# Optimization experiments

Measured on AMD Instinct MI355X. Metric: run time of the kernel, lower is better.

Reference implementation:

```python
import jax, jax.numpy as jnp
import numpy as np

EMB = 128
HEADS = 8
B = 8
T = 2048


def setup_inputs() -> dict:
    key = jax.random.key(0)
    ks = jax.random.split(key, 6)
    x = jax.random.normal(ks[0], (B, T, EMB), dtype=jnp.float32)
    # torch Linear(emb, heads*emb, bias=False): store as (in, out) so y = x @ W
    scale = 1.0 / np.sqrt(EMB)
    Wq = jax.random.uniform(ks[1], (EMB, HEADS * EMB), jnp.float32, -scale, scale)
    Wk = jax.random.uniform(ks[2], (EMB, HEADS * EMB), jnp.float32, -scale, scale)
    Wv = jax.random.uniform(ks[3], (EMB, HEADS * EMB), jnp.float32, -scale, scale)
    so = 1.0 / np.sqrt(HEADS * EMB)
    Wo = jax.random.uniform(ks[4], (HEADS * EMB, EMB), jnp.float32, -so, so)
    bo = jax.random.uniform(ks[5], (EMB,), jnp.float32, -so, so)
    return {"x": x, "Wq": Wq, "Wk": Wk, "Wv": Wv, "Wo": Wo, "bo": bo}


def reference(x, Wq, Wk, Wv, Wo, bo):
    b, t, e = x.shape
    h = HEADS
    q = (x @ Wq).reshape(b, t, h, e)  # [b,t,h,e]
    k = (x @ Wk).reshape(b, t, h, e)
    v = (x @ Wv).reshape(b, t, h, e)
    # scores: [b,h,q,k], scaled by sqrt(e) (per-head dim == emb here)
    scores = jnp.einsum('bqhe,bkhe->bhqk', q, k) / jnp.sqrt(jnp.asarray(e, x.dtype))
    attn = jax.nn.softmax(scores, axis=-1)
    out = jnp.einsum('bhqk,bkhe->bqhe', attn, v).reshape(b, t, h * e)
    return out @ Wo + bo
```

## Files before the change

kernel.cpp:

```cpp
#include <hip/hip_runtime.h>

using bf16x8 = __attribute__((ext_vector_type(8))) short;
using f32x4  = __attribute__((ext_vector_type(4))) float;
using f32x16 = __attribute__((ext_vector_type(16))) float;

__device__ __forceinline__ ushort f2bf(float f) {
    union { float f; unsigned int u; } c; c.f = f;
    unsigned int u = c.u;
    u = (u + 0x7fffu + ((u >> 16) & 1u)) >> 16;
    return (ushort)u;
}

#if defined(__has_builtin)
#if __has_builtin(__builtin_amdgcn_cvt_pk_bf16_f32)
#define HAS_PK_BF16 1
#endif
#if __has_builtin(__builtin_amdgcn_permlane32_swap)
#define HAS_PL32 1
#endif
#endif
__device__ __forceinline__ unsigned int pkbf(float a, float b) {
#ifdef HAS_PK_BF16
    typedef __bf16 bf2 __attribute__((ext_vector_type(2)));
    union { bf2 v; unsigned int u; } cv;
    cv.v = __builtin_amdgcn_cvt_pk_bf16_f32(a, b);
    return cv.u;
#else
    return (unsigned int)f2bf(a) | ((unsigned int)f2bf(b) << 16);
#endif
}

__device__ __forceinline__ void pl32swap(unsigned &a, unsigned &b) {
#ifdef HAS_PL32
    typedef unsigned uint2v __attribute__((ext_vector_type(2)));
    uint2v r = __builtin_amdgcn_permlane32_swap(a, b, false, false);
    a = r.x; b = r.y;
#else
    asm volatile("v_permlane32_swap_b32 %0, %1" : "+v"(a), "+v"(b));
#endif
}

__device__ __forceinline__ void dma16(const ushort* g, ushort* l) {
    __builtin_amdgcn_global_load_lds(
        (const __attribute__((address_space(1))) unsigned int*)g,
        (__attribute__((address_space(3))) unsigned int*)l, 16, 0, 0);
}

constexpr int BB   = 8;
constexpr int HH   = 8;
constexpr int TT   = 2048;
constexpr int DD   = 128;
#define C2F (0.08838834764831845f * 1.4426950408889634f)

__global__ void prep_kernel(const float* __restrict__ x,
                            const float* __restrict__ Wq, const float* __restrict__ Wk,
                            const float* __restrict__ Wv, const float* __restrict__ Wo,
                            ushort* __restrict__ xb, ushort* __restrict__ WqkvT,
                            ushort* __restrict__ WoT) {
    int t = blockIdx.x * 256 + threadIdx.x;
    if (t < 524288) {
        float4 v = ((const float4*)x)[t];
        ushort4 o;
        o.x = f2bf(v.x); o.y = f2bf(v.y); o.z = f2bf(v.z); o.w = f2bf(v.w);
        ((ushort4*)xb)[t] = o;
    } else if (t < 524288 + 393216) {
        int i = t - 524288;
        int j = i >> 7, kk = i & 127;
        const float* W = (j < 1024) ? Wq : ((j < 2048) ? Wk : Wv);
        int jj = j & 1023;
        WqkvT[j * 128 + kk] = f2bf(W[kk * 1024 + jj]);
    } else {
        int i = t - 917504;
        int e = i >> 10, kk = i & 1023;
        WoT[e * 1024 + kk] = f2bf(Wo[kk * 128 + e]);
    }
}

__global__ __launch_bounds__(256, 2)
void qkv_gemm(const ushort* __restrict__ xb, const ushort* __restrict__ WqkvT,
              ushort* __restrict__ q, ushort* __restrict__ k, ushort* __restrict__ vt) {
    __shared__ ushort Al[128 * 136];
    __shared__ ushort Bl[128 * 136];
    const int tid = threadIdx.x;
    const int n0 = blockIdx.x * 128, m0 = blockIdx.y * 128;

    for (int s = tid; s < 2048; s += 256) {
        int row = s >> 4, oct = s & 15;
        *(uint4*)&Al[row * 136 + oct * 8] = *(const uint4*)&xb[m0 * 128 + s * 8];
        *(uint4*)&Bl[row * 136 + oct * 8] = *(const uint4*)&WqkvT[n0 * 128 + s * 8];
    }
    __syncthreads();

    const int w = tid >> 6, lane = tid & 63, l15 = lane & 15, g = lane >> 4;
    const int wm = (w & 1) * 64, wn = (w >> 1) * 64;
    f32x4 acc[4][4] = {};

#pragma unroll
    for (int ks = 0; ks < 4; ks++) {
        bf16x8 af[4], bfr[4];
#pragma unroll
        for (int mb = 0; mb < 4; mb++)
            af[mb] = *(const bf16x8*)&Al[(wm + mb * 16 + l15) * 136 + ks * 32 + g * 8];
#pragma unroll
        for (int nb = 0; nb < 4; nb++)
            bfr[nb] = *(const bf16x8*)&Bl[(wn + nb * 16 + l15) * 136 + ks * 32 + g * 8];
#pragma unroll
        for (int mb = 0; mb < 4; mb++)
#pragma unroll
            for (int nb = 0; nb < 4; nb++)
                acc[mb][nb] = __builtin_amdgcn_mfma_f32_16x16x32_bf16(af[mb], bfr[nb], acc[mb][nb], 0, 0, 0);
    }

    const int which = n0 >> 10;
    const int b = m0 >> 11;
    const int h = (n0 >> 7) & 7;
    const int bh = b * HH + h;
    if (which == 0) {
#pragma unroll
        for (int mb = 0; mb < 4; mb++)
#pragma unroll
            for (int nb = 0; nb < 4; nb++)
#pragma unroll
                for (int r = 0; r < 4; r++) {
                    int t = (m0 + wm + mb * 16 + g * 4 + r) & 2047;
                    int e = wn + nb * 16 + l15;
                    q[((size_t)bh * TT + t) * DD + e] = f2bf(acc[mb][nb][r] * C2F);
                }
    } else if (which == 1) {
#pragma unroll
        for (int mb = 0; mb < 4; mb++)
#pragma unroll
            for (int nb = 0; nb < 4; nb++)
#pragma unroll
                for (int r = 0; r < 4; r++) {
                    int t = (m0 + wm + mb * 16 + g * 4 + r) & 2047;
                    int e = wn + nb * 16 + l15;
                    int esw = ((((e >> 3) ^ (t & 7)) << 3) | (e & 7));
                    k[((size_t)bh * TT + t) * DD + esw] = f2bf(acc[mb][nb][r]);
                }
    } else {
        __syncthreads();
        ushort* Tl = Al;
#pragma unroll
        for (int mb = 0; mb < 4; mb++)
#pragma unroll
            for (int nb = 0; nb < 4; nb++)
#pragma unroll
                for (int r = 0; r < 4; r++)
                    Tl[(wn + nb * 16 + l15) * 136 + wm + mb * 16 + g * 4 + r] = f2bf(acc[mb][nb][r]);
        __syncthreads();
        const int c0 = (m0 & 2047) >> 5;
        for (int s = tid; s < 2048; s += 256) {
            int e = s >> 4, x = s & 15;
            int cl = x >> 2, pos = x & 3;
            int el = e & 15;
            int vsw = (el ^ (el >> 2)) & 3;
            int tsrc = cl * 32 + ((pos ^ vsw) * 8);
            uint4 val = *(const uint4*)&Tl[e * 136 + tsrc];
            *(uint4*)&vt[(size_t)(((bh * 64 + c0 + cl) * 128) + e) * 32 + pos * 8] = val;
        }
    }
}

__global__ __launch_bounds__(256, 3)
void attn_kernel(const ushort* __restrict__ q, const ushort* __restrict__ k,
                 const ushort* __restrict__ vt, ushort* __restrict__ ao) {
    __shared__ ushort Kl[3][32 * 128];
    __shared__ ushort Vl[3][128 * 32];

    const int idx = blockIdx.x;
    const int h = idx & 7, b = (idx >> 3) & 7, qt128 = idx >> 6;
    const int t0 = qt128 * 128;
    const int bh = b * HH + h;
    const ushort* qg  = q  + (size_t)bh * TT * DD;
    const ushort* kg  = k  + (size_t)bh * TT * DD;
    const ushort* vtg = vt + (size_t)bh * 64 * DD * 32;

    const int tid = threadIdx.x, w = tid >> 6, lane = tid & 63;
    const int l31 = lane & 31, hi = lane >> 5, l15 = lane & 15;
    const int swk = lane & 7;
    const int swv = (l15 ^ (l15 >> 2)) & 3;

    bf16x8 qf[8];
#pragma unroll
    for (int ks = 0; ks < 8; ks++)
        qf[ks] = *(const bf16x8*)&qg[(size_t)(t0 + w * 32 + l31) * DD + ks * 16 + hi * 8];

    const int seg = tid * 8;
#pragma unroll
    for (int pc = 0; pc < 2; pc++)
#pragma unroll
        for (int j = 0; j < 2; j++) {
            dma16(kg  + (size_t)pc * 4096 + seg + j * 2048, &Kl[pc][seg + j * 2048]);
            dma16(vtg + (size_t)pc * 4096 + seg + j * 2048, &Vl[pc][seg + j * 2048]);
        }

    f32x16 o[4] = {};
    float ls = 0.0f;

    int cur = 0, nxt = 2;
    for (int c = 0; c < 64; c++) {
        if (c < 63) asm volatile("s_waitcnt vmcnt(4)" ::: "memory");
        else        asm volatile("s_waitcnt vmcnt(0)" ::: "memory");
        __builtin_amdgcn_s_barrier();
        __builtin_amdgcn_sched_barrier(0);

        bf16x8 kf[8];
#pragma unroll
        for (int ks = 0; ks < 8; ks++)
            kf[ks] = *(const bf16x8*)&Kl[cur][l31 * 128 + (((ks * 2 + hi) ^ swk) * 8)];
        if (c < 62) {
            const ushort* kn = kg + (size_t)(c + 2) * 4096;
#pragma unroll
            for (int j = 0; j < 2; j++)
                dma16(kn + seg + j * 2048, &Kl[nxt][seg + j * 2048]);
        }
        __builtin_amdgcn_s_barrier();
        asm volatile("s_waitcnt lgkmcnt(0)" ::: "memory");
        __builtin_amdgcn_sched_barrier(0);
        f32x16 st = {};
        __builtin_amdgcn_s_setprio(1);
#pragma unroll
        for (int ks = 0; ks < 8; ks++)
            st = __builtin_amdgcn_mfma_f32_32x32x16_bf16(kf[ks], qf[ks], st, 0, 0, 0);
        __builtin_amdgcn_s_setprio(0);
        __builtin_amdgcn_s_barrier();

        float p[16];
#pragma unroll
        for (int r = 0; r < 16; r++) p[r] = __builtin_amdgcn_exp2f(st[r]);
        ls += (((p[0] + p[1]) + (p[2] + p[3])) + ((p[4] + p[5]) + (p[6] + p[7])))
            + (((p[8] + p[9]) + (p[10] + p[11])) + ((p[12] + p[13]) + (p[14] + p[15])));
        unsigned a0 = pkbf(p[0],  p[1]),  a1 = pkbf(p[2],  p[3]);
        unsigned a2 = pkbf(p[4],  p[5]),  a3 = pkbf(p[6],  p[7]);
        unsigned a4 = pkbf(p[8],  p[9]),  a5 = pkbf(p[10], p[11]);
        unsigned a6 = pkbf(p[12], p[13]), a7 = pkbf(p[14], p[15]);
        pl32swap(a0, a2); pl32swap(a1, a3);
        pl32swap(a4, a6); pl32swap(a5, a7);
        union { unsigned u[4]; bf16x8 v; } A, B;
        A.u[0] = a0; A.u[1] = a1; A.u[2] = a2; A.u[3] = a3;
        B.u[0] = a4; B.u[1] = a5; B.u[2] = a6; B.u[3] = a7;
        bf16x8 paA = A.v, paB = B.v;

        bf16x8 vb[8];
#pragma unroll
        for (int et = 0; et < 4; et++)
#pragma unroll
            for (int ks2 = 0; ks2 < 2; ks2++)
                vb[et * 2 + ks2] = *(const bf16x8*)&Vl[cur][(et * 32 + l31) * 32 + (((ks2 * 2 + hi) ^ swv) * 8)];
        if (c < 62) {
            const ushort* vn = vtg + (size_t)(c + 2) * 4096;
#pragma unroll
            for (int j = 0; j < 2; j++)
                dma16(vn + seg + j * 2048, &Vl[nxt][seg + j * 2048]);
        }
        __builtin_amdgcn_s_barrier();
        asm volatile("s_waitcnt lgkmcnt(0)" ::: "memory");
        __builtin_amdgcn_sched_barrier(0);
        __builtin_amdgcn_s_setprio(1);
#pragma unroll
        for (int et = 0; et < 4; et++) {
            o[et] = __builtin_amdgcn_mfma_f32_32x32x16_bf16(paA, vb[et * 2 + 0], o[et], 0, 0, 0);
            o[et] = __builtin_amdgcn_mfma_f32_32x32x16_bf16(paB, vb[et * 2 + 1], o[et], 0, 0, 0);
        }
        __builtin_amdgcn_s_setprio(0);

        cur = (cur == 2) ? 0 : cur + 1;
        nxt = (nxt == 2) ? 0 : nxt + 1;
    }

    float tot = ls + __shfl_xor(ls, 32);
    const size_t aobase = (size_t)(b * TT) * 1024 + h * 128;
#pragma unroll
    for (int r = 0; r < 16; r++) {
        int ql = (r & 3) + 8 * (r >> 2) + 4 * hi;
        float inv = 1.0f / __shfl(tot, ql, 64);
        int m = t0 + w * 32 + ql;
#pragma unroll
        for (int et = 0; et < 4; et++)
            ao[aobase + (size_t)m * 1024 + et * 32 + l31] = f2bf(o[et][r] * inv);
    }
}

__global__ __launch_bounds__(256, 2)
void outproj_gemm(const ushort* __restrict__ ao, const ushort* __restrict__ WoT,
                  const float* __restrict__ bo, float* __restrict__ out) {
    __shared__ ushort Al[64 * 72];
    __shared__ ushort Bl[64 * 72];
    const int tid = threadIdx.x;
    const int n0 = blockIdx.x * 64, m0 = blockIdx.y * 64;
    const int w = tid >> 6, lane = tid & 63, l15 = lane & 15, g = lane >> 4;
    const int wm = (w & 1) * 32, wn = (w >> 1) * 32;
    f32x4 acc[2][2] = {};

    for (int kc = 0; kc < 16; kc++) {
        int k0 = kc * 64;
        __syncthreads();
        for (int s = tid; s < 512; s += 256) {
            int row = s >> 3, oct = s & 7;
            *(uint4*)&Al[row * 72 + oct * 8] = *(const uint4*)&ao[(size_t)(m0 + row) * 1024 + k0 + oct * 8];
            *(uint4*)&Bl[row * 72 + oct * 8] = *(const uint4*)&WoT[(n0 + row) * 1024 + k0 + oct * 8];
        }
        __syncthreads();
#pragma unroll
        for (int ks = 0; ks < 2; ks++) {
            bf16x8 af[2], bfr[2];
#pragma unroll
            for (int mb = 0; mb < 2; mb++)
                af[mb] = *(const bf16x8*)&Al[(wm + mb * 16 + l15) * 72 + ks * 32 + g * 8];
#pragma unroll
            for (int nb = 0; nb < 2; nb++)
                bfr[nb] = *(const bf16x8*)&Bl[(wn + nb * 16 + l15) * 72 + ks * 32 + g * 8];
#pragma unroll
            for (int mb = 0; mb < 2; mb++)
#pragma unroll
                for (int nb = 0; nb < 2; nb++)
                    acc[mb][nb] = __builtin_amdgcn_mfma_f32_16x16x32_bf16(af[mb], bfr[nb], acc[mb][nb], 0, 0, 0);
        }
    }

#pragma unroll
    for (int mb = 0; mb < 2; mb++)
#pragma unroll
        for (int nb = 0; nb < 2; nb++) {
            int j = n0 + wn + nb * 16 + l15;
            float bias = bo[j];
#pragma unroll
            for (int r = 0; r < 4; r++) {
                int m = m0 + wm + mb * 16 + g * 4 + r;
                out[(size_t)m * 128 + j] = acc[mb][nb][r] + bias;
            }
        }
}

extern "C" void kernel_launch(void* const* d_in, const int* in_sizes, int n_in,
                              void* d_out, int out_size, void* d_ws, size_t ws_size,
                              hipStream_t stream) {
    const float* x  = (const float*)d_in[0];
    const float* Wq = (const float*)d_in[1];
    const float* Wk = (const float*)d_in[2];
    const float* Wv = (const float*)d_in[3];
    const float* Wo = (const float*)d_in[4];
    const float* bo = (const float*)d_in[5];
    float* out = (float*)d_out;

    char* ws = (char*)d_ws;
    ushort* xb    = (ushort*)(ws);
    ushort* WqkvT = (ushort*)(ws + 4194304);
    ushort* WoT   = (ushort*)(ws + 4980736);
    ushort* qb    = (ushort*)(ws + 5242880);
    ushort* kb    = (ushort*)(ws + 38797312);
    ushort* vtb   = (ushort*)(ws + 72351744);
    ushort* ao    = (ushort*)(ws + 105906176);

    prep_kernel<<<4096, 256, 0, stream>>>(x, Wq, Wk, Wv, Wo, xb, WqkvT, WoT);
    qkv_gemm<<<dim3(24, 128), 256, 0, stream>>>(xb, WqkvT, qb, kb, vtb);
    attn_kernel<<<1024, 256, 0, stream>>>(qb, kb, vtb, ao);
    outproj_gemm<<<dim3(2, 256), 256, 0, stream>>>(ao, WoT, bo, out);
}
```

Before: 267.7 us.

## Tile weight transposes, stage Q/K stores through LDS, pipeline out-projection GEMM

The prep kernel now transposes the Q/K/V and output weights through 32x32 LDS tiles, so reads and writes are coalesced and vectorized instead of strided scalar accesses. In the QKV GEMM, the Q and K epilogues stage results in LDS and write 16-byte rows, with the K swizzle applied per octet, replacing scattered 2-byte stores. The output-projection GEMM is rewritten as 32x128 tiles with a three-stage global_load_lds DMA pipeline and XOR-swizzled LDS. That pipeline overlaps loads with MFMA and reads each ao row only once, at the cost of extra barriers and more LDS per block.

```diff
diff --git a/kernel.cpp b/kernel.cpp
--- a/kernel.cpp
+++ b/kernel.cpp
@@ -57,22 +57,41 @@
                             const float* __restrict__ Wv, const float* __restrict__ Wo,
                             ushort* __restrict__ xb, ushort* __restrict__ WqkvT,
                             ushort* __restrict__ WoT) {
-    int t = blockIdx.x * 256 + threadIdx.x;
-    if (t < 524288) {
+    const int bid = blockIdx.x, tid = threadIdx.x;
+    if (bid < 2048) {
+        int t = bid * 256 + tid;
         float4 v = ((const float4*)x)[t];
         ushort4 o;
         o.x = f2bf(v.x); o.y = f2bf(v.y); o.z = f2bf(v.z); o.w = f2bf(v.w);
         ((ushort4*)xb)[t] = o;
-    } else if (t < 524288 + 393216) {
-        int i = t - 524288;
-        int j = i >> 7, kk = i & 127;
-        const float* W = (j < 1024) ? Wq : ((j < 2048) ? Wk : Wv);
-        int jj = j & 1023;
-        WqkvT[j * 128 + kk] = f2bf(W[kk * 1024 + jj]);
+        return;
+    }
+    __shared__ ushort T[32][33];
+    const int r = tid >> 3, c4 = (tid & 7) * 4;
+    if (bid < 2432) {
+        int tile = bid - 2048;
+        int mat = tile >> 7;
+        int tt = tile & 127;
+        int kt = tt >> 5, jt = tt & 31;
+        const float* W = (mat == 0) ? Wq : ((mat == 1) ? Wk : Wv);
+        float4 v = *(const float4*)&W[(size_t)(kt * 32 + r) * 1024 + jt * 32 + c4];
+        T[r][c4 + 0] = f2bf(v.x); T[r][c4 + 1] = f2bf(v.y);
+        T[r][c4 + 2] = f2bf(v.z); T[r][c4 + 3] = f2bf(v.w);
+        __syncthreads();
+        ushort4 o;
+        o.x = T[c4 + 0][r]; o.y = T[c4 + 1][r]; o.z = T[c4 + 2][r]; o.w = T[c4 + 3][r];
+        int j = mat * 1024 + jt * 32 + r;
+        *(ushort4*)&WqkvT[(size_t)j * 128 + kt * 32 + c4] = o;
     } else {
-        int i = t - 917504;
-        int e = i >> 10, kk = i & 1023;
-        WoT[e * 1024 + kk] = f2bf(Wo[kk * 128 + e]);
+        int tile = bid - 2432;
+        int kt = tile >> 2, et = tile & 3;
+        float4 v = *(const float4*)&Wo[(size_t)(kt * 32 + r) * 128 + et * 32 + c4];
+        T[r][c4 + 0] = f2bf(v.x); T[r][c4 + 1] = f2bf(v.y);
+        T[r][c4 + 2] = f2bf(v.z); T[r][c4 + 3] = f2bf(v.w);
+        __syncthreads();
+        ushort4 o;
+        o.x = T[c4 + 0][r]; o.y = T[c4 + 1][r]; o.z = T[c4 + 2][r]; o.w = T[c4 + 3][r];
+        *(ushort4*)&WoT[(size_t)(et * 32 + r) * 1024 + kt * 32 + c4] = o;
     }
 }
 
@@ -115,29 +134,33 @@
     const int b = m0 >> 11;
     const int h = (n0 >> 7) & 7;
     const int bh = b * HH + h;
-    if (which == 0) {
+    if (which != 2) {
+        __syncthreads();
+        ushort* Tl = Al;
+        const float sc = (which == 0) ? C2F : 1.0f;
 #pragma unroll
         for (int mb = 0; mb < 4; mb++)
 #pragma unroll
             for (int nb = 0; nb < 4; nb++)
 #pragma unroll
-                for (int r = 0; r < 4; r++) {
-                    int t = (m0 + wm + mb * 16 + g * 4 + r) & 2047;
-                    int e = wn + nb * 16 + l15;
-                    q[((size_t)bh * TT + t) * DD + e] = f2bf(acc[mb][nb][r] * C2F);
-                }
-    } else if (which == 1) {
-#pragma unroll
-        for (int mb = 0; mb < 4; mb++)
-#pragma unroll
-            for (int nb = 0; nb < 4; nb++)
-#pragma unroll
-                for (int r = 0; r < 4; r++) {
-                    int t = (m0 + wm + mb * 16 + g * 4 + r) & 2047;
-                    int e = wn + nb * 16 + l15;
-                    int esw = ((((e >> 3) ^ (t & 7)) << 3) | (e & 7));
-                    k[((size_t)bh * TT + t) * DD + esw] = f2bf(acc[mb][nb][r]);
-                }
+                for (int r = 0; r < 4; r++)
+                    Tl[(wm + mb * 16 + g * 4 + r) * 136 + wn + nb * 16 + l15] = f2bf(acc[mb][nb][r] * sc);
+        __syncthreads();
+        const int tb = m0 & 2047;
+        if (which == 0) {
+            for (int s = tid; s < 2048; s += 256) {
+                int row = s >> 4, oct = s & 15;
+                uint4 val = *(const uint4*)&Tl[row * 136 + oct * 8];
+                *(uint4*)&q[((size_t)bh * TT + tb + row) * DD + oct * 8] = val;
+            }
+        } else {
+            for (int s = tid; s < 2048; s += 256) {
+                int row = s >> 4, oct = s & 15;
+                uint4 val = *(const uint4*)&Tl[row * 136 + oct * 8];
+                int t = tb + row;
+                *(uint4*)&k[((size_t)bh * TT + t) * DD + ((oct ^ (t & 7)) * 8)] = val;
+            }
+        }
     } else {
         __syncthreads();
         ushort* Tl = Al;
@@ -285,32 +308,60 @@
 __global__ __launch_bounds__(256, 2)
 void outproj_gemm(const ushort* __restrict__ ao, const ushort* __restrict__ WoT,
                   const float* __restrict__ bo, float* __restrict__ out) {
-    __shared__ ushort Al[64 * 72];
-    __shared__ ushort Bl[64 * 72];
+    __shared__ ushort Aol[3][32 * 64];
+    __shared__ ushort Bol[3][128 * 64];
     const int tid = threadIdx.x;
-    const int n0 = blockIdx.x * 64, m0 = blockIdx.y * 64;
-    const int w = tid >> 6, lane = tid & 63, l15 = lane & 15, g = lane >> 4;
-    const int wm = (w & 1) * 32, wn = (w >> 1) * 32;
+    const int m0 = blockIdx.x * 32;
+    const int lane = tid & 63, w = tid >> 6, l15 = lane & 15, g = lane >> 4;
+    const int wn = w * 32;
+
+    const int srow = tid >> 3, sblk = tid & 7;
+    const int sao = (m0 + srow) * 1024 + ((sblk ^ (srow & 7)) * 8);
+
+    {
+#pragma unroll
+        for (int pc = 0; pc < 2; pc++) {
+            dma16(&ao[(size_t)(sao + pc * 64)], &Aol[pc][tid * 8]);
+#pragma unroll
+            for (int j = 0; j < 4; j++) {
+                int u = j * 256 + tid, row = u >> 3, blk = u & 7;
+                dma16(&WoT[(size_t)row * 1024 + pc * 64 + ((blk ^ (row & 7)) * 8)], &Bol[pc][u * 8]);
+            }
+        }
+    }
+
     f32x4 acc[2][2] = {};
-
     for (int kc = 0; kc < 16; kc++) {
-        int k0 = kc * 64;
-        __syncthreads();
-        for (int s = tid; s < 512; s += 256) {
-            int row = s >> 3, oct = s & 7;
-            *(uint4*)&Al[row * 72 + oct * 8] = *(const uint4*)&ao[(size_t)(m0 + row) * 1024 + k0 + oct * 8];
-            *(uint4*)&Bl[row * 72 + oct * 8] = *(const uint4*)&WoT[(n0 + row) * 1024 + k0 + oct * 8];
-        }
-        __syncthreads();
+        if (kc < 15) asm volatile("s_waitcnt vmcnt(5) lgkmcnt(0)" ::: "memory");
+        else         asm volatile("s_waitcnt vmcnt(0) lgkmcnt(0)" ::: "memory");
+        __builtin_amdgcn_s_barrier();
+        __builtin_amdgcn_sched_barrier(0);
+
+        if (kc < 14) {
+            int slot = (kc + 2) % 3, k0 = (kc + 2) * 64;
+            dma16(&ao[(size_t)(sao + k0)], &Aol[slot][tid * 8]);
+#pragma unroll
+            for (int j = 0; j < 4; j++) {
+                int u = j * 256 + tid, row = u >> 3, blk = u & 7;
+                dma16(&WoT[(size_t)row * 1024 + k0 + ((blk ^ (row & 7)) * 8)], &Bol[slot][u * 8]);
+            }
+        }
+
+        const ushort* Ac = Aol[kc % 3];
+        const ushort* Bc = Bol[kc % 3];
 #pragma unroll
         for (int ks = 0; ks < 2; ks++) {
             bf16x8 af[2], bfr[2];
 #pragma unroll
-            for (int mb = 0; mb < 2; mb++)
-                af[mb] = *(const bf16x8*)&Al[(wm + mb * 16 + l15) * 72 + ks * 32 + g * 8];
-#pragma unroll
-            for (int nb = 0; nb < 2; nb++)
-                bfr[nb] = *(const bf16x8*)&Bl[(wn + nb * 16 + l15) * 72 + ks * 32 + g * 8];
+            for (int mb = 0; mb < 2; mb++) {
+                int row = mb * 16 + l15;
+                af[mb] = *(const bf16x8*)&Ac[row * 64 + (((ks * 4 + g) ^ (row & 7)) * 8)];
+            }
+#pragma unroll
+            for (int nb = 0; nb < 2; nb++) {
+                int rb = wn + nb * 16 + l15;
+                bfr[nb] = *(const bf16x8*)&Bc[rb * 64 + (((ks * 4 + g) ^ (rb & 7)) * 8)];
+            }
 #pragma unroll
             for (int mb = 0; mb < 2; mb++)
 #pragma unroll
@@ -323,11 +374,11 @@
     for (int mb = 0; mb < 2; mb++)
 #pragma unroll
         for (int nb = 0; nb < 2; nb++) {
-            int j = n0 + wn + nb * 16 + l15;
+            int j = wn + nb * 16 + l15;
             float bias = bo[j];
 #pragma unroll
             for (int r = 0; r < 4; r++) {
-                int m = m0 + wm + mb * 16 + g * 4 + r;
+                int m = m0 + mb * 16 + g * 4 + r;
                 out[(size_t)m * 128 + j] = acc[mb][nb][r] + bias;
             }
         }
@@ -353,8 +404,8 @@
     ushort* vtb   = (ushort*)(ws + 72351744);
     ushort* ao    = (ushort*)(ws + 105906176);
 
-    prep_kernel<<<4096, 256, 0, stream>>>(x, Wq, Wk, Wv, Wo, xb, WqkvT, WoT);
+    prep_kernel<<<2560, 256, 0, stream>>>(x, Wq, Wk, Wv, Wo, xb, WqkvT, WoT);
     qkv_gemm<<<dim3(24, 128), 256, 0, stream>>>(xb, WqkvT, qb, kb, vtb);
     attn_kernel<<<1024, 256, 0, stream>>>(qb, kb, vtb, ao);
-    outproj_gemm<<<dim3(2, 256), 256, 0, stream>>>(ao, WoT, bo, out);
-}
+    outproj_gemm<<<512, 256, 0, stream>>>(ao, WoT, bo, out);
+}
```

New measurement: 271.0 us. About the same (+1.2%).
